# Kernel tuning notes

Hardware: AMD Instinct MI355X
Metric: run time of the kernel (lower is better)

Reference implementation:

```python
import jax, jax.numpy as jnp
from jax import lax
import numpy as np
import math

DIM = 96      # channels
HEADS = 3     # num_heads
WS = 8        # window size
SHIFT = 4     # window_size // 2 (depth is odd -> shifted)
TLC = 64      # tlc_kernel
H = 264
W = 264


def _grid_idxes(h, w, k1, k2):
    # Faithful replication of the torch grids() tiling index logic (static ints).
    num_row = (h - 1) // k1 + 1
    num_col = (w - 1) // k2 + 1
    step_j = k2 if num_col == 1 else math.ceil((w - k2) / (num_col - 1) - 1e-8)
    step_i = k1 if num_row == 1 else math.ceil((h - k1) / (num_row - 1) - 1e-8)
    idxes = []
    i = 0
    last_i = False
    while i < h and not last_i:
        j = 0
        if i + k1 >= h:
            i = h - k1
            last_i = True
        last_j = False
        while j < w and not last_j:
            if j + k2 >= w:
                j = w - k2
                last_j = True
            idxes.append((i, j))
            j = j + step_j
        i = i + step_i
    return idxes


def setup_inputs() -> dict:
    key = jax.random.key(0)
    ks = jax.random.split(key, 4)
    return {
        "x": jax.random.normal(ks[0], (1, DIM, H, W), jnp.float32),
        "temperature": jnp.ones((HEADS, 1, 1), jnp.float32),
        "qkv_w": jax.random.normal(ks[1], (3 * DIM, DIM), jnp.float32) * 0.05,
        "dw_w": jax.random.normal(ks[2], (3 * DIM, 1, 3, 3), jnp.float32) * 0.1,
        "proj_w": jax.random.normal(ks[3], (DIM, DIM), jnp.float32) * 0.05,
    }


def reference(x, temperature, qkv_w, dw_w, proj_w):
    b, c, h, w = x.shape
    # depth % 2 == 1 -> cyclic shift
    x = jnp.roll(x, (-SHIFT, -SHIFT), axis=(2, 3))
    # 1x1 pointwise conv (no bias)
    qkv = jnp.einsum('oc,bchw->bohw', qkv_w, x)
    # 3x3 depthwise conv, padding 1
    qkv = lax.conv_general_dilated(
        qkv, dw_w, window_strides=(1, 1), padding=[(1, 1), (1, 1)],
        feature_group_count=3 * c, dimension_numbers=('NCHW', 'OIHW', 'NCHW'))
    # --- TLC grids: overlapping tiles (eval path, b == 1) ---
    k1, k2 = min(h, TLC), min(w, TLC)
    idxes = _grid_idxes(h, w, k1, k2)
    parts = jnp.concatenate([qkv[:, :, i:i + k1, j:j + k2] for (i, j) in idxes], axis=0)  # [T,3c,k1,k2]
    T, C3, th, tw = parts.shape
    nh, nw = th // WS, tw // WS
    # window partition: b c (h b0) (w b1) -> (b h w) c b0 b1 -> flatten spatial
    win = parts.reshape(T, C3, nh, WS, nw, WS).transpose(0, 2, 4, 1, 3, 5)
    win = win.reshape(T * nh * nw, C3, WS * WS)  # [Bw, 3c, 64]
    q, k, v = jnp.split(win, 3, axis=1)  # each [Bw, c, 64]
    ch = c // HEADS
    q = q.reshape(-1, HEADS, ch, WS * WS)
    k = k.reshape(-1, HEADS, ch, WS * WS)
    v = v.reshape(-1, HEADS, ch, WS * WS)
    # L2 normalize along token dim (F.normalize eps=1e-12)
    q = q / jnp.maximum(jnp.linalg.norm(q, axis=-1, keepdims=True), 1e-12)
    k = k / jnp.maximum(jnp.linalg.norm(k, axis=-1, keepdims=True), 1e-12)
    # channel attention: [Bw, head, ch, ch]
    attn = jax.nn.relu(jnp.einsum('bhcn,bhdn->bhcd', q, k) * temperature)
    out = jnp.einsum('bhcd,bhdn->bhcn', attn, v)  # [Bw, head, ch, 64]
    out = out.reshape(-1, c, WS, WS)
    # window merge back to tiles
    out = out.reshape(T, nh, nw, c, WS, WS).transpose(0, 3, 1, 4, 2, 5).reshape(T, c, th, tw)
    # --- TLC grids_inverse: scatter-add overlapping tiles and average ---
    preds = jnp.zeros((b, c, h, w), x.dtype)
    cnt = np.zeros((h, w), np.float32)
    for t, (i, j) in enumerate(idxes):
        preds = preds.at[0, :, i:i + k1, j:j + k2].add(out[t])
        cnt[i:i + k1, j:j + k2] += 1.0
    preds = preds / jnp.asarray(cnt)
    # 1x1 output projection
    out = jnp.einsum('oc,bchw->bohw', proj_w, preds)
    # undo cyclic shift
    return jnp.roll(out, (SHIFT, SHIFT), axis=(2, 3))
```

## Files before the change

kernel.cpp:

```cpp
#include <hip/hip_runtime.h>
#include <hip/hip_bf16.h>

#define HW_ 69696
#define W_ 264
#define H_ 264

typedef short bf16x8 __attribute__((ext_vector_type(8)));
typedef float f32x4 __attribute__((ext_vector_type(4)));

static __device__ __forceinline__ unsigned short f2b(float f) {
  __hip_bfloat16 h = __float2bfloat16(f);
  return *reinterpret_cast<unsigned short*>(&h);
}
static __device__ __forceinline__ float b2f(unsigned short u) {
  __hip_bfloat16 h;
  *reinterpret_cast<unsigned short*>(&h) = u;
  return __bfloat162float(h);
}
static __device__ __forceinline__ float lo_f(unsigned int u) {
  union { unsigned int i; float f; } c; c.i = u << 16; return c.f;
}
static __device__ __forceinline__ float hi_f(unsigned int u) {
  union { unsigned int i; float f; } c; c.i = u & 0xffff0000u; return c.f;
}

__global__ __launch_bounds__(256, 5) void k_gemm(const float* __restrict__ x,
                                                 const float* __restrict__ w,
                                                 unsigned short* __restrict__ outb) {
  __shared__ __align__(16) unsigned short As[96 * 104];

  const int tid = threadIdx.x;
  const int wid = tid >> 6, lane = tid & 63;
  const int quad = lane >> 4, lo = lane & 15;
  const int px0 = blockIdx.x * 64;
  const int px = px0 + wid * 16 + lo;

  const int y = px / W_, xx = px - y * W_;
  int y2 = y + 4; if (y2 >= H_) y2 -= H_;
  int x2 = xx + 4; if (x2 >= W_) x2 -= W_;
  const float* xb = x + y2 * W_ + x2;

  bf16x8 bfv[3];
#pragma unroll
  for (int ks = 0; ks < 3; ++ks) {
    const float* xp = xb + (size_t)(ks * 32 + quad * 8) * HW_;
    float f[8];
#pragma unroll
    for (int i = 0; i < 8; ++i) f[i] = xp[(size_t)i * HW_];
    union { bf16x8 v; unsigned short s[8]; } u;
#pragma unroll
    for (int i = 0; i < 8; ++i) u.s[i] = f2b(f[i]);
    bfv[ks] = u.v;
  }

  for (int oc = 0; oc < 3; ++oc) {
    __syncthreads();
    const float* wp = w + oc * 96 * 96;
    for (int l = tid; l < 96 * 24; l += 256) {
      int o = l / 24, c4 = (l - (l / 24) * 24) * 4;
      float4 v = *(const float4*)&wp[o * 96 + c4];
      unsigned int p0 = (unsigned int)f2b(v.x) | ((unsigned int)f2b(v.y) << 16);
      unsigned int p1 = (unsigned int)f2b(v.z) | ((unsigned int)f2b(v.w) << 16);
      *(uint2*)&As[o * 104 + c4] = make_uint2(p0, p1);
    }
    __syncthreads();

    f32x4 acc[6];
#pragma unroll
    for (int mt = 0; mt < 6; ++mt) acc[mt] = {0.f, 0.f, 0.f, 0.f};
#pragma unroll
    for (int ks = 0; ks < 3; ++ks) {
      const int kb = ks * 32 + quad * 8;
#pragma unroll
      for (int mt = 0; mt < 6; ++mt) {
        bf16x8 a = *(const bf16x8*)&As[(mt * 16 + lo) * 104 + kb];
        acc[mt] = __builtin_amdgcn_mfma_f32_16x16x32_bf16(a, bfv[ks], acc[mt], 0, 0, 0);
      }
    }

#pragma unroll
    for (int mt = 0; mt < 6; ++mt) {
      const int u = oc * 12 + 2 * mt + (quad >> 1);
      unsigned int p0 = (unsigned int)f2b(acc[mt][0]) | ((unsigned int)f2b(acc[mt][1]) << 16);
      unsigned int p1 = (unsigned int)f2b(acc[mt][2]) | ((unsigned int)f2b(acc[mt][3]) << 16);
      *(uint2*)((char*)outb + ((size_t)u * HW_ + px) * 16 + (quad & 1) * 8) = make_uint2(p0, p1);
    }
  }
}

__global__ __launch_bounds__(256, 3) void k_dwattn(const unsigned short* __restrict__ qkvb,
                                                   const float* __restrict__ dwv,
                                                   const float* __restrict__ temp,
                                                   unsigned short* __restrict__ tout) {
  __shared__ __align__(16) char smem[49024];
  unsigned short* qkS = (unsigned short*)smem;
  unsigned short* vS = (unsigned short*)(smem + 27648);
  uint4* stgBase = (uint4*)(smem + 40960);
  unsigned short* attnL = (unsigned short*)(smem + 40960);
  float* invn = (float*)(smem + 48640);
  unsigned short* Cs = (unsigned short*)smem;

  const int tid = threadIdx.x;
  const int wi = ((blockIdx.x & 7) << 3) | (blockIdx.x >> 3);
  const int t = blockIdx.y;
  const int i0 = (t / 5) * 50, j0 = (t % 5) * 50;
  const int wy = wi >> 3, wx = wi & 7;
  const int gy0 = i0 + wy * 8, gx0 = j0 + wx * 8;

  const int h = tid >> 6, lane = tid & 63;
  const int w_ = __builtin_amdgcn_readfirstlane(h);
  const int quad = lane >> 4, lo = lane & 15;

  {
    uint4* stgW = stgBase + w_ * 100;
    const int r0 = lane >> 3, c0 = lane & 7;
    const int sy0 = lane / 10, sx0 = lane - sy0 * 10;
    const int ii1 = lane + 64;
    const int sy1 = ii1 / 10, sx1 = ii1 - sy1 * 10;
    const int gyA = gy0 - 1 + sy0, gxA = gx0 - 1 + sx0;
    const int gyB = gy0 - 1 + sy1, gxB = gx0 - 1 + sx1;
    const bool okA = (unsigned)gyA < (unsigned)H_ && (unsigned)gxA < (unsigned)W_;
    const bool okB = ii1 < 100 && (unsigned)gyB < (unsigned)H_ && (unsigned)gxB < (unsigned)W_;
    const size_t offA = (size_t)gyA * W_ + gxA;
    const size_t offB = (size_t)gyB * W_ + gxB;
    const uint4* qb4 = (const uint4*)qkvb;

    uint4 vA[9], vB[9];
#pragma unroll
    for (int k = 0; k < 9; ++k) {
      const int u = k * 4 + w_;
      vA[k] = okA ? qb4[(size_t)u * HW_ + offA] : make_uint4(0u, 0u, 0u, 0u);
      vB[k] = okB ? qb4[(size_t)u * HW_ + offB] : make_uint4(0u, 0u, 0u, 0u);
    }

#pragma unroll
    for (int k = 0; k < 9; ++k) {
      const int u = k * 4 + w_;
      stgW[lane] = vA[k];
      if (ii1 < 100) stgW[ii1] = vB[k];
      asm volatile("s_waitcnt lgkmcnt(0)" ::: "memory");
      __builtin_amdgcn_sched_barrier(0);

      const float* wp = dwv + u * 72;
      float acc[8] = {0.f, 0.f, 0.f, 0.f, 0.f, 0.f, 0.f, 0.f};
#pragma unroll
      for (int dy = 0; dy < 3; ++dy)
#pragma unroll
        for (int dx = 0; dx < 3; ++dx) {
          uint4 v = stgW[(r0 + dy) * 10 + (c0 + dx)];
          float w0 = wp[0 * 9 + dy * 3 + dx], w1 = wp[1 * 9 + dy * 3 + dx];
          float w2 = wp[2 * 9 + dy * 3 + dx], w3 = wp[3 * 9 + dy * 3 + dx];
          float w4 = wp[4 * 9 + dy * 3 + dx], w5 = wp[5 * 9 + dy * 3 + dx];
          float w6 = wp[6 * 9 + dy * 3 + dx], w7 = wp[7 * 9 + dy * 3 + dx];
          acc[0] += w0 * lo_f(v.x); acc[1] += w1 * hi_f(v.x);
          acc[2] += w2 * lo_f(v.y); acc[3] += w3 * hi_f(v.y);
          acc[4] += w4 * lo_f(v.z); acc[5] += w5 * hi_f(v.z);
          acc[6] += w6 * lo_f(v.w); acc[7] += w7 * hi_f(v.w);
        }
      if (k < 6) {
#pragma unroll
        for (int i = 0; i < 8; ++i)
          qkS[(u * 8 + i) * 72 + lane] = f2b(acc[i]);
      } else {
        uint4 o;
        o.x = (unsigned int)f2b(acc[0]) | ((unsigned int)f2b(acc[1]) << 16);
        o.y = (unsigned int)f2b(acc[2]) | ((unsigned int)f2b(acc[3]) << 16);
        o.z = (unsigned int)f2b(acc[4]) | ((unsigned int)f2b(acc[5]) << 16);
        o.w = (unsigned int)f2b(acc[6]) | ((unsigned int)f2b(acc[7]) << 16);
        *(uint4*)&vS[lane * 104 + (u - 24) * 8] = o;
      }
    }
  }
  __syncthreads();

  const int cb = h * 32;
  f32x4 S[2][2];
  bf16x8 qf[2][2], kf[2][2];
  float ivk[2];
  if (h < 3) {
#pragma unroll
    for (int mt = 0; mt < 2; ++mt)
#pragma unroll
      for (int kt = 0; kt < 2; ++kt) {
        const int row = cb + mt * 16 + lo;
        const int pxc = (kt * 4 + quad) * 8;
        qf[mt][kt] = *(const bf16x8*)&qkS[row * 72 + pxc];
        kf[mt][kt] = *(const bf16x8*)&qkS[(96 + row) * 72 + pxc];
      }

#pragma unroll
    for (int mt = 0; mt < 2; ++mt)
#pragma unroll
      for (int nt = 0; nt < 2; ++nt) {
        S[mt][nt] = {0.f, 0.f, 0.f, 0.f};
#pragma unroll
        for (int kt = 0; kt < 2; ++kt)
          S[mt][nt] = __builtin_amdgcn_mfma_f32_16x16x32_bf16(qf[mt][kt], kf[nt][kt], S[mt][nt], 0, 0, 0);
      }

#pragma unroll
    for (int mt = 0; mt < 2; ++mt) {
      float sq = 0.f, sk = 0.f;
#pragma unroll
      for (int kt = 0; kt < 2; ++kt)
#pragma unroll
        for (int j = 0; j < 8; ++j) {
          float a = b2f((unsigned short)qf[mt][kt][j]);
          float b = b2f((unsigned short)kf[mt][kt][j]);
          sq += a * a;
          sk += b * b;
        }
      sq += __shfl_xor(sq, 16);
      sq += __shfl_xor(sq, 32);
      sk += __shfl_xor(sk, 16);
      sk += __shfl_xor(sk, 32);
      if (quad == 0) invn[h * 32 + mt * 16 + lo] = 1.f / fmaxf(sqrtf(sq), 1e-12f);
      ivk[mt] = 1.f / fmaxf(sqrtf(sk), 1e-12f);
    }
  }
  __syncthreads();

  if (h < 3) {
    const float ts = temp[h];
#pragma unroll
    for (int mt = 0; mt < 2; ++mt)
#pragma unroll
      for (int nt = 0; nt < 2; ++nt)
#pragma unroll
        for (int r = 0; r < 4; ++r) {
          int c = mt * 16 + quad * 4 + r;
          float v = S[mt][nt][r] * invn[h * 32 + c] * ivk[nt] * ts;
          attnL[(h * 32 + c) * 40 + nt * 16 + lo] = f2b(fmaxf(v, 0.f));
        }
  }
  __syncthreads();

  f32x4 O[2][4];
  if (h < 3) {
    bf16x8 af[2];
#pragma unroll
    for (int mt = 0; mt < 2; ++mt)
      af[mt] = *(const bf16x8*)&attnL[(h * 32 + mt * 16 + lo) * 40 + quad * 8];

    const int uv = h * 4 + quad;
#pragma unroll
    for (int nt = 0; nt < 4; ++nt) {
      const int px = nt * 16 + lo;
      uint4 vraw = *(const uint4*)&vS[px * 104 + uv * 8];
      bf16x8 vf = *reinterpret_cast<bf16x8*>(&vraw);
#pragma unroll
      for (int mt = 0; mt < 2; ++mt) {
        f32x4 z = {0.f, 0.f, 0.f, 0.f};
        O[mt][nt] = __builtin_amdgcn_mfma_f32_16x16x32_bf16(af[mt], vf, z, 0, 0, 0);
      }
    }
  }
  __syncthreads();

  if (h < 3) {
#pragma unroll
    for (int mt = 0; mt < 2; ++mt)
#pragma unroll
      for (int nt = 0; nt < 4; ++nt) {
        const int px = nt * 16 + lo;
        unsigned int p0 = (unsigned int)f2b(O[mt][nt][0]) | ((unsigned int)f2b(O[mt][nt][1]) << 16);
        unsigned int p1 = (unsigned int)f2b(O[mt][nt][2]) | ((unsigned int)f2b(O[mt][nt][3]) << 16);
        *(uint2*)&Cs[px * 104 + cb + mt * 16 + quad * 4] = make_uint2(p0, p1);
      }
  }
  __syncthreads();

  for (int idx = tid; idx < 64 * 12; idx += 256) {
    int u = idx >> 6, rec = idx & 63;
    int r = rec >> 3, j = rec & 7;
    size_t local = (size_t)(wy * 8 + r) * 64 + wx * 8 + j;
    ((uint4*)tout)[((size_t)t * 12 + u) * 4096 + local] = ((const uint4*)(Cs + rec * 104))[u];
  }
}

__global__ __launch_bounds__(256, 5) void k_avgproj(const float* __restrict__ w,
                                                    const unsigned short* __restrict__ tout,
                                                    float* __restrict__ outf) {
  __shared__ __align__(16) unsigned short As[96 * 104];
  const int tid = threadIdx.x;
  const int wid = tid >> 6, lane = tid & 63;
  const int quad = lane >> 4, lo = lane & 15;
  const int px0 = blockIdx.x * 64;
  const int px = px0 + wid * 16 + lo;

  for (int l = tid; l < 96 * 24; l += 256) {
    int o = l / 24, c4 = (l - (l / 24) * 24) * 4;
    float4 v = *(const float4*)&w[o * 96 + c4];
    unsigned int p0 = (unsigned int)f2b(v.x) | ((unsigned int)f2b(v.y) << 16);
    unsigned int p1 = (unsigned int)f2b(v.z) | ((unsigned int)f2b(v.w) << 16);
    *(uint2*)&As[o * 104 + c4] = make_uint2(p0, p1);
  }

  const int y = px / W_, xx = px - y * W_;
  int loy = (y >= 64) ? (y - 14) / 50 : 0;
  int hiy = y / 50; if (hiy > 4) hiy = 4;
  int lox = (xx >= 64) ? (xx - 14) / 50 : 0;
  int hix = xx / 50; if (hix > 4) hix = 4;
  float a24[24];
#pragma unroll
  for (int i = 0; i < 24; ++i) a24[i] = 0.f;
  int cnt = 0;
  for (int ty = loy; ty <= hiy; ++ty)
    for (int tx = lox; tx <= hix; ++tx) {
      size_t local = (size_t)((y - ty * 50) << 6) + (xx - tx * 50);
      const uint4* rp = (const uint4*)tout +
                        ((size_t)(ty * 5 + tx) * 12 + quad) * 4096 + local;
#pragma unroll
      for (int ks = 0; ks < 3; ++ks) {
        uint4 v = rp[(size_t)ks * 4 * 4096];
        a24[ks * 8 + 0] += lo_f(v.x); a24[ks * 8 + 1] += hi_f(v.x);
        a24[ks * 8 + 2] += lo_f(v.y); a24[ks * 8 + 3] += hi_f(v.y);
        a24[ks * 8 + 4] += lo_f(v.z); a24[ks * 8 + 5] += hi_f(v.z);
        a24[ks * 8 + 6] += lo_f(v.w); a24[ks * 8 + 7] += hi_f(v.w);
      }
      ++cnt;
    }
  const float inv = 1.f / (float)cnt;
  bf16x8 bfv[3];
#pragma unroll
  for (int ks = 0; ks < 3; ++ks) {
    union { bf16x8 v; unsigned short s[8]; } u;
#pragma unroll
    for (int i = 0; i < 8; ++i) u.s[i] = f2b(a24[ks * 8 + i] * inv);
    bfv[ks] = u.v;
  }
  __syncthreads();

  f32x4 acc[6];
#pragma unroll
  for (int mt = 0; mt < 6; ++mt) acc[mt] = {0.f, 0.f, 0.f, 0.f};
#pragma unroll
  for (int ks = 0; ks < 3; ++ks) {
    const int kb = ks * 32 + quad * 8;
#pragma unroll
    for (int mt = 0; mt < 6; ++mt) {
      bf16x8 a = *(const bf16x8*)&As[(mt * 16 + lo) * 104 + kb];
      acc[mt] = __builtin_amdgcn_mfma_f32_16x16x32_bf16(a, bfv[ks], acc[mt], 0, 0, 0);
    }
  }

  {
    int y2 = y + 4; if (y2 >= H_) y2 -= H_;
    int x2 = xx + 4; if (x2 >= W_) x2 -= W_;
    int tp = y2 * W_ + x2;
#pragma unroll
    for (int mt = 0; mt < 6; ++mt) {
      int row = mt * 16 + quad * 4;
#pragma unroll
      for (int r = 0; r < 4; ++r)
        outf[(size_t)(row + r) * HW_ + tp] = acc[mt][r];
    }
  }
}

extern "C" void kernel_launch(void* const* d_in, const int* in_sizes, int n_in,
                              void* d_out, int out_size, void* d_ws, size_t ws_size,
                              hipStream_t stream) {
  (void)in_sizes; (void)n_in; (void)out_size; (void)ws_size;
  const float* x = (const float*)d_in[0];
  const float* temp = (const float*)d_in[1];
  const float* qkvw = (const float*)d_in[2];
  const float* dww = (const float*)d_in[3];
  const float* projw = (const float*)d_in[4];
  float* out = (float*)d_out;

  char* ws = (char*)d_ws;
  const size_t SZQ = (size_t)288 * HW_ * 2;
  unsigned short* qkvb = (unsigned short*)ws;
  unsigned short* tout = (unsigned short*)(ws + SZQ);

  k_gemm<<<dim3(1089), 256, 0, stream>>>(x, qkvw, qkvb);
  k_dwattn<<<dim3(64, 25), 256, 0, stream>>>(qkvb, dww, temp, tout);
  k_avgproj<<<dim3(1089), 256, 0, stream>>>(projw, tout, out);
}
```

Measured before the change: 147.0 us.

## Give each wave its own head in dwattn, drop block barriers and LDS staging

The fused depthwise-conv plus window-attention kernel now runs with 192 threads, and each wave owns one head end to end. Each wave computes its own q/k/v depthwise channels in a private LDS region, so block-wide __syncthreads are replaced by per-wave waitcnt fences. The output is written directly from MFMA registers to global memory instead of through an LDS transpose. Global loads are now software-pipelined one step ahead rather than all issued up front, which cuts register pressure. The trade-off is less memory-level parallelism per wave and narrower (8-byte) scattered global stores.

```diff
diff --git a/kernel.cpp b/kernel.cpp
--- a/kernel.cpp
+++ b/kernel.cpp
@@ -88,31 +88,32 @@
   }
 }
 
-__global__ __launch_bounds__(256, 3) void k_dwattn(const unsigned short* __restrict__ qkvb,
+#define PW 16000
+__global__ __launch_bounds__(192, 2) void k_dwattn(const unsigned short* __restrict__ qkvb,
                                                    const float* __restrict__ dwv,
                                                    const float* __restrict__ temp,
                                                    unsigned short* __restrict__ tout) {
-  __shared__ __align__(16) char smem[49024];
-  unsigned short* qkS = (unsigned short*)smem;
-  unsigned short* vS = (unsigned short*)(smem + 27648);
-  uint4* stgBase = (uint4*)(smem + 40960);
-  unsigned short* attnL = (unsigned short*)(smem + 40960);
-  float* invn = (float*)(smem + 48640);
-  unsigned short* Cs = (unsigned short*)smem;
+  __shared__ __align__(16) char smem[3 * PW];
 
   const int tid = threadIdx.x;
+  const int h = tid >> 6, lane = tid & 63;
+  const int w_ = __builtin_amdgcn_readfirstlane(h);
+  const int quad = lane >> 4, lo = lane & 15;
+
+  char* wbase = smem + w_ * PW;
+  unsigned short* qk = (unsigned short*)wbase;
+  unsigned short* vp = (unsigned short*)(wbase + 9216);
+  uint4* stg = (uint4*)(wbase + 13312);
+  unsigned short* attnL = (unsigned short*)(wbase + 13312);
+  float* invn = (float*)(wbase + 15872);
+
   const int wi = ((blockIdx.x & 7) << 3) | (blockIdx.x >> 3);
   const int t = blockIdx.y;
   const int i0 = (t / 5) * 50, j0 = (t % 5) * 50;
   const int wy = wi >> 3, wx = wi & 7;
   const int gy0 = i0 + wy * 8, gx0 = j0 + wx * 8;
 
-  const int h = tid >> 6, lane = tid & 63;
-  const int w_ = __builtin_amdgcn_readfirstlane(h);
-  const int quad = lane >> 4, lo = lane & 15;
-
   {
-    uint4* stgW = stgBase + w_ * 100;
     const int r0 = lane >> 3, c0 = lane & 7;
     const int sy0 = lane / 10, sx0 = lane - sy0 * 10;
     const int ii1 = lane + 64;
@@ -125,19 +126,20 @@
     const size_t offB = (size_t)gyB * W_ + gxB;
     const uint4* qb4 = (const uint4*)qkvb;
 
-    uint4 vA[9], vB[9];
-#pragma unroll
-    for (int k = 0; k < 9; ++k) {
-      const int u = k * 4 + w_;
-      vA[k] = okA ? qb4[(size_t)u * HW_ + offA] : make_uint4(0u, 0u, 0u, 0u);
-      vB[k] = okB ? qb4[(size_t)u * HW_ + offB] : make_uint4(0u, 0u, 0u, 0u);
-    }
-
-#pragma unroll
-    for (int k = 0; k < 9; ++k) {
-      const int u = k * 4 + w_;
-      stgW[lane] = vA[k];
-      if (ii1 < 100) stgW[ii1] = vB[k];
+    const int u0 = w_ * 4;
+    uint4 vA = okA ? qb4[(size_t)u0 * HW_ + offA] : make_uint4(0u, 0u, 0u, 0u);
+    uint4 vB = okB ? qb4[(size_t)u0 * HW_ + offB] : make_uint4(0u, 0u, 0u, 0u);
+
+#pragma unroll
+    for (int i = 0; i < 12; ++i) {
+      const int u = (i >> 2) * 12 + u0 + (i & 3);
+      stg[lane] = vA;
+      if (ii1 < 100) stg[ii1] = vB;
+      if (i < 11) {
+        const int un = ((i + 1) >> 2) * 12 + u0 + ((i + 1) & 3);
+        vA = okA ? qb4[(size_t)un * HW_ + offA] : make_uint4(0u, 0u, 0u, 0u);
+        vB = okB ? qb4[(size_t)un * HW_ + offB] : make_uint4(0u, 0u, 0u, 0u);
+      }
       asm volatile("s_waitcnt lgkmcnt(0)" ::: "memory");
       __builtin_amdgcn_sched_barrier(0);
 
@@ -147,7 +149,7 @@
       for (int dy = 0; dy < 3; ++dy)
 #pragma unroll
         for (int dx = 0; dx < 3; ++dx) {
-          uint4 v = stgW[(r0 + dy) * 10 + (c0 + dx)];
+          uint4 v = stg[(r0 + dy) * 10 + (c0 + dx)];
           float w0 = wp[0 * 9 + dy * 3 + dx], w1 = wp[1 * 9 + dy * 3 + dx];
           float w2 = wp[2 * 9 + dy * 3 + dx], w3 = wp[3 * 9 + dy * 3 + dx];
           float w4 = wp[4 * 9 + dy * 3 + dx], w5 = wp[5 * 9 + dy * 3 + dx];
@@ -157,71 +159,69 @@
           acc[4] += w4 * lo_f(v.z); acc[5] += w5 * hi_f(v.z);
           acc[6] += w6 * lo_f(v.w); acc[7] += w7 * hi_f(v.w);
         }
-      if (k < 6) {
-#pragma unroll
-        for (int i = 0; i < 8; ++i)
-          qkS[(u * 8 + i) * 72 + lane] = f2b(acc[i]);
+      if (i < 8) {
+#pragma unroll
+        for (int ch = 0; ch < 8; ++ch)
+          qk[(i * 8 + ch) * 72 + lane] = f2b(acc[ch]);
       } else {
         uint4 o;
         o.x = (unsigned int)f2b(acc[0]) | ((unsigned int)f2b(acc[1]) << 16);
         o.y = (unsigned int)f2b(acc[2]) | ((unsigned int)f2b(acc[3]) << 16);
         o.z = (unsigned int)f2b(acc[4]) | ((unsigned int)f2b(acc[5]) << 16);
         o.w = (unsigned int)f2b(acc[6]) | ((unsigned int)f2b(acc[7]) << 16);
-        *(uint4*)&vS[lane * 104 + (u - 24) * 8] = o;
-      }
-    }
-  }
-  __syncthreads();
-
-  const int cb = h * 32;
+        *(uint4*)&vp[((i - 8) * 64 + lane) * 8] = o;
+      }
+    }
+  }
+  asm volatile("s_waitcnt lgkmcnt(0)" ::: "memory");
+  __builtin_amdgcn_sched_barrier(0);
+
+  bf16x8 qf[2][2], kf[2][2];
+#pragma unroll
+  for (int mt = 0; mt < 2; ++mt)
+#pragma unroll
+    for (int kt = 0; kt < 2; ++kt) {
+      const int pxc = (kt * 4 + quad) * 8;
+      qf[mt][kt] = *(const bf16x8*)&qk[(mt * 16 + lo) * 72 + pxc];
+      kf[mt][kt] = *(const bf16x8*)&qk[(32 + mt * 16 + lo) * 72 + pxc];
+    }
+
   f32x4 S[2][2];
-  bf16x8 qf[2][2], kf[2][2];
+#pragma unroll
+  for (int mt = 0; mt < 2; ++mt)
+#pragma unroll
+    for (int nt = 0; nt < 2; ++nt) {
+      S[mt][nt] = {0.f, 0.f, 0.f, 0.f};
+#pragma unroll
+      for (int kt = 0; kt < 2; ++kt)
+        S[mt][nt] = __builtin_amdgcn_mfma_f32_16x16x32_bf16(qf[mt][kt], kf[nt][kt], S[mt][nt], 0, 0, 0);
+    }
+
   float ivk[2];
-  if (h < 3) {
-#pragma unroll
-    for (int mt = 0; mt < 2; ++mt)
-#pragma unroll
-      for (int kt = 0; kt < 2; ++kt) {
-        const int row = cb + mt * 16 + lo;
-        const int pxc = (kt * 4 + quad) * 8;
-        qf[mt][kt] = *(const bf16x8*)&qkS[row * 72 + pxc];
-        kf[mt][kt] = *(const bf16x8*)&qkS[(96 + row) * 72 + pxc];
-      }
-
-#pragma unroll
-    for (int mt = 0; mt < 2; ++mt)
-#pragma unroll
-      for (int nt = 0; nt < 2; ++nt) {
-        S[mt][nt] = {0.f, 0.f, 0.f, 0.f};
-#pragma unroll
-        for (int kt = 0; kt < 2; ++kt)
-          S[mt][nt] = __builtin_amdgcn_mfma_f32_16x16x32_bf16(qf[mt][kt], kf[nt][kt], S[mt][nt], 0, 0, 0);
-      }
-
-#pragma unroll
-    for (int mt = 0; mt < 2; ++mt) {
-      float sq = 0.f, sk = 0.f;
-#pragma unroll
-      for (int kt = 0; kt < 2; ++kt)
-#pragma unroll
-        for (int j = 0; j < 8; ++j) {
-          float a = b2f((unsigned short)qf[mt][kt][j]);
-          float b = b2f((unsigned short)kf[mt][kt][j]);
-          sq += a * a;
-          sk += b * b;
-        }
-      sq += __shfl_xor(sq, 16);
-      sq += __shfl_xor(sq, 32);
-      sk += __shfl_xor(sk, 16);
-      sk += __shfl_xor(sk, 32);
-      if (quad == 0) invn[h * 32 + mt * 16 + lo] = 1.f / fmaxf(sqrtf(sq), 1e-12f);
-      ivk[mt] = 1.f / fmaxf(sqrtf(sk), 1e-12f);
-    }
-  }
-  __syncthreads();
-
-  if (h < 3) {
-    const float ts = temp[h];
+#pragma unroll
+  for (int mt = 0; mt < 2; ++mt) {
+    float sq = 0.f, sk = 0.f;
+#pragma unroll
+    for (int kt = 0; kt < 2; ++kt)
+#pragma unroll
+      for (int j = 0; j < 8; ++j) {
+        float a = b2f((unsigned short)qf[mt][kt][j]);
+        float b = b2f((unsigned short)kf[mt][kt][j]);
+        sq += a * a;
+        sk += b * b;
+      }
+    sq += __shfl_xor(sq, 16);
+    sq += __shfl_xor(sq, 32);
+    sk += __shfl_xor(sk, 16);
+    sk += __shfl_xor(sk, 32);
+    if (quad == 0) invn[mt * 16 + lo] = 1.f / fmaxf(sqrtf(sq), 1e-12f);
+    ivk[mt] = 1.f / fmaxf(sqrtf(sk), 1e-12f);
+  }
+  asm volatile("s_waitcnt lgkmcnt(0)" ::: "memory");
+  __builtin_amdgcn_sched_barrier(0);
+
+  {
+    const float ts = temp[w_];
 #pragma unroll
     for (int mt = 0; mt < 2; ++mt)
 #pragma unroll
@@ -229,52 +229,43 @@
 #pragma unroll
         for (int r = 0; r < 4; ++r) {
           int c = mt * 16 + quad * 4 + r;
-          float v = S[mt][nt][r] * invn[h * 32 + c] * ivk[nt] * ts;
-          attnL[(h * 32 + c) * 40 + nt * 16 + lo] = f2b(fmaxf(v, 0.f));
+          float v = S[mt][nt][r] * invn[c] * ivk[nt] * ts;
+          attnL[c * 40 + nt * 16 + lo] = f2b(fmaxf(v, 0.f));
         }
   }
-  __syncthreads();
+  asm volatile("s_waitcnt lgkmcnt(0)" ::: "memory");
+  __builtin_amdgcn_sched_barrier(0);
+
+  bf16x8 af[2];
+#pragma unroll
+  for (int mt = 0; mt < 2; ++mt)
+    af[mt] = *(const bf16x8*)&attnL[(mt * 16 + lo) * 40 + quad * 8];
 
   f32x4 O[2][4];
-  if (h < 3) {
-    bf16x8 af[2];
-#pragma unroll
-    for (int mt = 0; mt < 2; ++mt)
-      af[mt] = *(const bf16x8*)&attnL[(h * 32 + mt * 16 + lo) * 40 + quad * 8];
-
-    const int uv = h * 4 + quad;
+#pragma unroll
+  for (int nt = 0; nt < 4; ++nt) {
+    const int px = nt * 16 + lo;
+    uint4 vraw = *(const uint4*)&vp[(quad * 64 + px) * 8];
+    bf16x8 vf = *reinterpret_cast<bf16x8*>(&vraw);
+#pragma unroll
+    for (int mt = 0; mt < 2; ++mt) {
+      f32x4 z = {0.f, 0.f, 0.f, 0.f};
+      O[mt][nt] = __builtin_amdgcn_mfma_f32_16x16x32_bf16(af[mt], vf, z, 0, 0, 0);
+    }
+  }
+
+#pragma unroll
+  for (int mt = 0; mt < 2; ++mt) {
+    const int u = w_ * 4 + mt * 2 + (quad >> 1);
 #pragma unroll
     for (int nt = 0; nt < 4; ++nt) {
       const int px = nt * 16 + lo;
-      uint4 vraw = *(const uint4*)&vS[px * 104 + uv * 8];
-      bf16x8 vf = *reinterpret_cast<bf16x8*>(&vraw);
-#pragma unroll
-      for (int mt = 0; mt < 2; ++mt) {
-        f32x4 z = {0.f, 0.f, 0.f, 0.f};
-        O[mt][nt] = __builtin_amdgcn_mfma_f32_16x16x32_bf16(af[mt], vf, z, 0, 0, 0);
-      }
-    }
-  }
-  __syncthreads();
-
-  if (h < 3) {
-#pragma unroll
-    for (int mt = 0; mt < 2; ++mt)
-#pragma unroll
-      for (int nt = 0; nt < 4; ++nt) {
-        const int px = nt * 16 + lo;
-        unsigned int p0 = (unsigned int)f2b(O[mt][nt][0]) | ((unsigned int)f2b(O[mt][nt][1]) << 16);
-        unsigned int p1 = (unsigned int)f2b(O[mt][nt][2]) | ((unsigned int)f2b(O[mt][nt][3]) << 16);
-        *(uint2*)&Cs[px * 104 + cb + mt * 16 + quad * 4] = make_uint2(p0, p1);
-      }
-  }
-  __syncthreads();
-
-  for (int idx = tid; idx < 64 * 12; idx += 256) {
-    int u = idx >> 6, rec = idx & 63;
-    int r = rec >> 3, j = rec & 7;
-    size_t local = (size_t)(wy * 8 + r) * 64 + wx * 8 + j;
-    ((uint4*)tout)[((size_t)t * 12 + u) * 4096 + local] = ((const uint4*)(Cs + rec * 104))[u];
+      const int local = (wy * 8 + (px >> 3)) * 64 + wx * 8 + (px & 7);
+      unsigned int p0 = (unsigned int)f2b(O[mt][nt][0]) | ((unsigned int)f2b(O[mt][nt][1]) << 16);
+      unsigned int p1 = (unsigned int)f2b(O[mt][nt][2]) | ((unsigned int)f2b(O[mt][nt][3]) << 16);
+      *(uint2*)((char*)tout + (((size_t)t * 12 + u) * 4096 + local) * 16 + (quad & 1) * 8) =
+          make_uint2(p0, p1);
+    }
   }
 }
 
@@ -375,6 +366,6 @@
   unsigned short* tout = (unsigned short*)(ws + SZQ);
 
   k_gemm<<<dim3(1089), 256, 0, stream>>>(x, qkvw, qkvb);
-  k_dwattn<<<dim3(64, 25), 256, 0, stream>>>(qkvb, dww, temp, tout);
+  k_dwattn<<<dim3(64, 25), 192, 0, stream>>>(qkvb, dww, temp, tout);
   k_avgproj<<<dim3(1089), 256, 0, stream>>>(projw, tout, out);
 }
```

Measured after the change: 147.8 us. Within noise of the previous version (+0.5%).
